# Kernel optimization log

Hardware: AMD Instinct MI355X
Metric: run time of the kernel (lower is better)

The kernel has to match this reference:

```python
import jax, jax.numpy as jnp
import numpy as np


def _ce(logits, labels):
    # per-element cross entropy; logits [N,C], labels [N] int
    logp = jax.nn.log_softmax(logits, axis=-1)
    return -jnp.take_along_axis(logp, labels[:, None].astype(jnp.int32), axis=1)[:, 0]


def _masked_mean(x, m):
    cnt = jnp.sum(m)
    return jnp.where(cnt > 0, jnp.sum(x * m) / jnp.maximum(cnt, 1.0), 0.0)


def _ohem(predict, target, train_mask, negative_ratio=3.0):
    # predict [N,2], target/train_mask [N] int {0,1}
    pos = (target * train_mask) > 0
    neg = ((1 - target) * train_mask) > 0
    n_pos = jnp.sum(pos).astype(jnp.float32)
    loss_all = _ce(predict, target)
    loss_pos = jnp.where(n_pos > 0, jnp.sum(jnp.where(pos, loss_all, 0.0)), 0.0)
    n_neg_total = jnp.sum(neg)
    n_neg = jnp.where(n_pos > 0,
                      jnp.minimum(n_neg_total, (negative_ratio * n_pos).astype(jnp.int32)),
                      jnp.minimum(100, n_neg_total))
    # hard-negative mining: top-n_neg of the per-pixel negative CE losses
    neg_sorted = jnp.sort(jnp.where(neg, loss_all, -jnp.inf))[::-1]
    loss_neg = jnp.sum(jnp.where(jnp.arange(neg_sorted.shape[0]) < n_neg, neg_sorted, 0.0))
    return (loss_pos + loss_neg) / (n_pos + n_neg.astype(jnp.float32))


def _forward(inputs, gcn_pred, gcn_labels, train_mask, tr_mask, tcl_mask, radii_map, sin_map, cos_map):
    B, C, H, W = inputs.shape
    ch = jnp.transpose(inputs, (0, 2, 3, 1)).reshape(-1, C)  # [N,8], N=B*H*W
    tr_pred = ch[:, 0:2]
    tcl_pred = ch[:, 2:4]
    sin_pred = ch[:, 4]
    cos_pred = ch[:, 5]
    scale = jnp.sqrt(1.0 / (sin_pred ** 2 + cos_pred ** 2 + 1e-4))
    sin_pred = sin_pred * scale
    cos_pred = cos_pred * scale
    top_pred = ch[:, 6]
    bot_pred = ch[:, 7]

    tm = train_mask.reshape(-1)
    tr = tr_mask.reshape(-1)
    tcl = tcl_mask[:, :, :, 0].reshape(-1)
    sin_t = sin_map.reshape(-1)
    cos_t = cos_map.reshape(-1)
    top_t = radii_map[:, :, :, 0].reshape(-1)
    bot_t = radii_map[:, :, :, 1].reshape(-1)

    # TR loss with OHEM hard-negative mining
    loss_tr = _ohem(tr_pred, tr, tm)

    # TCL loss: mean CE over train_mask*tr_mask positives
    tr_train = ((tm * tr) > 0).astype(jnp.float32)
    loss_tcl = _masked_mean(_ce(tcl_pred, tcl), tr_train)

    # geometry losses over tcl_mask pixels
    tclm = (tcl > 0).astype(jnp.float32)
    d_top = jnp.abs(top_pred / (top_t + 0.01) - 1.0)
    d_bot = jnp.abs(bot_pred / (bot_t + 0.01) - 1.0)
    sl_top = jnp.where(d_top < 1.0, 0.5 * d_top * d_top, d_top - 0.5)  # torch smooth_l1 (beta=1)
    sl_bot = jnp.where(d_bot < 1.0, 0.5 * d_bot * d_bot, d_bot - 0.5)
    loss_radii = _masked_mean(sl_top + sl_bot, tclm)

    sigma = 9.0
    d_sin = jnp.abs(sin_pred - sin_t)
    d_cos = jnp.abs(cos_pred - cos_t)
    sl_sin = jnp.where(d_sin < 1.0 / sigma, 0.5 * d_sin * d_sin * sigma, d_sin - 0.5 / sigma)
    sl_cos = jnp.where(d_cos < 1.0 / sigma, 0.5 * d_cos * d_cos * sigma, d_cos - 0.5 / sigma)
    loss_sin = _masked_mean(sl_sin, tclm)
    loss_cos = _masked_mean(sl_cos, tclm)

    gcn_loss = jnp.mean(_ce(gcn_pred, gcn_labels.reshape(-1)))
    return (loss_tr, loss_tcl, loss_sin, loss_cos, loss_radii, gcn_loss)


def setup_inputs() -> dict:
    key = jax.random.key(0)
    ks = jax.random.split(key, 9)
    B, H, W = 8, 640, 640
    return {
        'inputs': jax.random.normal(ks[0], (B, 8, H, W), dtype=jnp.float32),
        'gcn_pred': jax.random.normal(ks[1], (4096, 2), dtype=jnp.float32),
        'gcn_labels': jax.random.randint(ks[2], (4096,), 0, 2, dtype=jnp.int32),
        'train_mask': jax.random.randint(ks[3], (B, H, W), 0, 2, dtype=jnp.int32),
        'tr_mask': jax.random.randint(ks[4], (B, H, W), 0, 2, dtype=jnp.int32),
        'tcl_mask': jax.random.randint(ks[5], (B, H, W, 2), 0, 2, dtype=jnp.int32),
        'radii_map': jax.random.uniform(ks[6], (B, H, W, 2), dtype=jnp.float32),
        'sin_map': jax.random.normal(ks[7], (B, H, W), dtype=jnp.float32),
        'cos_map': jax.random.normal(ks[8], (B, H, W), dtype=jnp.float32),
    }


def reference(inputs, gcn_pred, gcn_labels, train_mask, tr_mask, tcl_mask, radii_map, sin_map, cos_map):
    return _forward(inputs, gcn_pred, gcn_labels, train_mask, tr_mask, tcl_mask, radii_map, sin_map, cos_map)
```

## Files before the change

### kernel.cpp

```cpp
#include <hip/hip_runtime.h>

#define HW_ 409600
#define NPIX 3276800
#define NB 4096
#define NGCN 4096
#define NBLK 2048

struct Ws {
  double sums[8];
  unsigned int cnts[8];
  unsigned int hcnt[NB];
  float hsum[NB];
  float pf[NBLK][8];
  unsigned int pc[NBLK][4];
};

__device__ __forceinline__ float ce2(float a0, float a1, int label) {
  float mx = fmaxf(a0, a1);
  float mn = fminf(a0, a1);
  float lse = mx + __logf(1.0f + __expf(mn - mx));
  return lse - (label ? a1 : a0);
}

__global__ __launch_bounds__(256) void k_init(Ws* ws) {
  int tid = threadIdx.x + blockIdx.x * blockDim.x;
  int nth = blockDim.x * gridDim.x;
  for (int i = tid; i < NB; i += nth) { ws->hcnt[i] = 0u; ws->hsum[i] = 0.f; }
}

__global__ __launch_bounds__(256) void k_main(
    const float* __restrict__ inp,
    const float* __restrict__ gcn_pred,
    const int* __restrict__ gcn_lab,
    const int* __restrict__ tmm,
    const int* __restrict__ trm,
    const int* __restrict__ tclm,
    const float* __restrict__ radm,
    const float* __restrict__ sinm,
    const float* __restrict__ cosm,
    Ws* __restrict__ ws) {
  float s_pos = 0.f, s_neg = 0.f, s_tcl = 0.f, s_sin = 0.f, s_cos = 0.f, s_rad = 0.f, s_gcn = 0.f;
  unsigned int c_pos = 0, c_neg = 0, c_tcl = 0;
  float mx_neg = 0.f;

  int tid = threadIdx.x + blockIdx.x * blockDim.x;
  int nth = blockDim.x * gridDim.x;

  if (tid < NGCN) {
    s_gcn = ce2(gcn_pred[2 * tid], gcn_pred[2 * tid + 1], gcn_lab[tid]);
  }

  const int ngrp = NPIX / 4;
  for (int g = tid; g < ngrp; g += nth) {
    int p = g * 4;
    int b = p / HW_;
    int q = p - b * HW_;
    const float* base = inp + (size_t)b * 8 * HW_ + q;
    float4 v0 = *(const float4*)(base);
    float4 v1 = *(const float4*)(base + HW_);
    float4 v2 = *(const float4*)(base + 2 * HW_);
    float4 v3 = *(const float4*)(base + 3 * HW_);
    float4 v4 = *(const float4*)(base + 4 * HW_);
    float4 v5 = *(const float4*)(base + 5 * HW_);
    float4 v6 = *(const float4*)(base + 6 * HW_);
    float4 v7 = *(const float4*)(base + 7 * HW_);
    int4 wtm = *(const int4*)(tmm + p);
    int4 wtr = *(const int4*)(trm + p);
    int4 tca = *(const int4*)(tclm + 2 * p);
    int4 tcb = *(const int4*)(tclm + 2 * p + 4);
    float4 ra = *(const float4*)(radm + 2 * p);
    float4 rb = *(const float4*)(radm + 2 * p + 4);
    float4 vs = *(const float4*)(sinm + p);
    float4 vc = *(const float4*)(cosm + p);

    float a0[4] = {v0.x, v0.y, v0.z, v0.w};
    float a1[4] = {v1.x, v1.y, v1.z, v1.w};
    float a2[4] = {v2.x, v2.y, v2.z, v2.w};
    float a3[4] = {v3.x, v3.y, v3.z, v3.w};
    float a4[4] = {v4.x, v4.y, v4.z, v4.w};
    float a5[4] = {v5.x, v5.y, v5.z, v5.w};
    float a6[4] = {v6.x, v6.y, v6.z, v6.w};
    float a7[4] = {v7.x, v7.y, v7.z, v7.w};
    int tmj[4] = {wtm.x, wtm.y, wtm.z, wtm.w};
    int trj[4] = {wtr.x, wtr.y, wtr.z, wtr.w};
    int tcj[4] = {tca.x, tca.z, tcb.x, tcb.z};
    float topt[4] = {ra.x, ra.z, rb.x, rb.z};
    float bott[4] = {ra.y, ra.w, rb.y, rb.w};
    float sint[4] = {vs.x, vs.y, vs.z, vs.w};
    float cost[4] = {vc.x, vc.y, vc.z, vc.w};

#pragma unroll
    for (int j = 0; j < 4; ++j) {
      bool pos = (trj[j] * tmj[j]) > 0;
      bool neg = ((1 - trj[j]) * tmj[j]) > 0;
      float ltr = ce2(a0[j], a1[j], trj[j]);
      if (pos) { s_pos += ltr; c_pos++; }
      if (neg) { s_neg += ltr; c_neg++; mx_neg = fmaxf(mx_neg, ltr); }
      float ltc = ce2(a2[j], a3[j], tcj[j]);
      if (pos) s_tcl += ltc;
      bool tc = tcj[j] > 0;
      float sp = a4[j], cp = a5[j];
      float sc = __builtin_amdgcn_rsqf(sp * sp + cp * cp + 1e-4f);
      sp *= sc; cp *= sc;
      float dsin = fabsf(sp - sint[j]);
      float dcos = fabsf(cp - cost[j]);
      const float inv9 = 1.f / 9.f;
      float slsin = dsin < inv9 ? 4.5f * dsin * dsin : dsin - 0.5f * inv9;
      float slcos = dcos < inv9 ? 4.5f * dcos * dcos : dcos - 0.5f * inv9;
      float dtop = fabsf(a6[j] * __builtin_amdgcn_rcpf(topt[j] + 0.01f) - 1.f);
      float dbot = fabsf(a7[j] * __builtin_amdgcn_rcpf(bott[j] + 0.01f) - 1.f);
      float sltop = dtop < 1.f ? 0.5f * dtop * dtop : dtop - 0.5f;
      float slbot = dbot < 1.f ? 0.5f * dbot * dbot : dbot - 0.5f;
      if (tc) { s_sin += slsin; s_cos += slcos; s_rad += sltop + slbot; c_tcl++; }
    }
  }

#pragma unroll
  for (int off = 32; off > 0; off >>= 1) {
    s_pos += __shfl_down(s_pos, off);
    s_neg += __shfl_down(s_neg, off);
    s_tcl += __shfl_down(s_tcl, off);
    s_sin += __shfl_down(s_sin, off);
    s_cos += __shfl_down(s_cos, off);
    s_rad += __shfl_down(s_rad, off);
    s_gcn += __shfl_down(s_gcn, off);
    c_pos += __shfl_down(c_pos, off);
    c_neg += __shfl_down(c_neg, off);
    c_tcl += __shfl_down(c_tcl, off);
    mx_neg = fmaxf(mx_neg, __shfl_down(mx_neg, off));
  }
  __shared__ float shf[4][8];
  __shared__ unsigned int shc[4][3];
  int wv = threadIdx.x >> 6, ln = threadIdx.x & 63;
  if (ln == 0) {
    shf[wv][0] = s_pos; shf[wv][1] = s_neg; shf[wv][2] = s_tcl; shf[wv][3] = s_sin;
    shf[wv][4] = s_cos; shf[wv][5] = s_rad; shf[wv][6] = s_gcn; shf[wv][7] = mx_neg;
    shc[wv][0] = c_pos; shc[wv][1] = c_neg; shc[wv][2] = c_tcl;
  }
  __syncthreads();
  if (threadIdx.x == 0) {
    float f0 = 0, f1 = 0, f2 = 0, f3 = 0, f4 = 0, f5 = 0, f6 = 0, f7 = 0;
    unsigned int u0 = 0, u1 = 0, u2 = 0;
#pragma unroll
    for (int w = 0; w < 4; ++w) {
      f0 += shf[w][0]; f1 += shf[w][1]; f2 += shf[w][2]; f3 += shf[w][3];
      f4 += shf[w][4]; f5 += shf[w][5]; f6 += shf[w][6];
      f7 = fmaxf(f7, shf[w][7]);
      u0 += shc[w][0]; u1 += shc[w][1]; u2 += shc[w][2];
    }
    ws->pf[blockIdx.x][0] = f0; ws->pf[blockIdx.x][1] = f1;
    ws->pf[blockIdx.x][2] = f2; ws->pf[blockIdx.x][3] = f3;
    ws->pf[blockIdx.x][4] = f4; ws->pf[blockIdx.x][5] = f5;
    ws->pf[blockIdx.x][6] = f6; ws->pf[blockIdx.x][7] = f7;
    ws->pc[blockIdx.x][0] = u0; ws->pc[blockIdx.x][1] = u1; ws->pc[blockIdx.x][2] = u2;
  }
}

__global__ __launch_bounds__(1024) void k_reduce(Ws* __restrict__ ws, float* __restrict__ out) {
  float f[8] = {0, 0, 0, 0, 0, 0, 0, 0};
  unsigned int u[3] = {0, 0, 0};
  int t = threadIdx.x;
#pragma unroll
  for (int rep = 0; rep < NBLK / 1024; ++rep) {
    int s = t + rep * 1024;
#pragma unroll
    for (int i = 0; i < 7; ++i) f[i] += ws->pf[s][i];
    f[7] = fmaxf(f[7], ws->pf[s][7]);
#pragma unroll
    for (int i = 0; i < 3; ++i) u[i] += ws->pc[s][i];
  }
#pragma unroll
  for (int off = 32; off > 0; off >>= 1) {
#pragma unroll
    for (int i = 0; i < 7; ++i) f[i] += __shfl_down(f[i], off);
    f[7] = fmaxf(f[7], __shfl_down(f[7], off));
#pragma unroll
    for (int i = 0; i < 3; ++i) u[i] += __shfl_down(u[i], off);
  }
  __shared__ float shf[16][8];
  __shared__ unsigned int shc[16][3];
  int wv = t >> 6, ln = t & 63;
  if (ln == 0) {
#pragma unroll
    for (int i = 0; i < 8; ++i) shf[wv][i] = f[i];
#pragma unroll
    for (int i = 0; i < 3; ++i) shc[wv][i] = u[i];
  }
  __syncthreads();
  if (t == 0) {
    double d[7] = {0, 0, 0, 0, 0, 0, 0};
    float mx = 0.f;
    unsigned int np = 0, nnt = 0, ntc = 0;
#pragma unroll
    for (int w = 0; w < 16; ++w) {
#pragma unroll
      for (int i = 0; i < 7; ++i) d[i] += (double)shf[w][i];
      mx = fmaxf(mx, shf[w][7]);
      np += shc[w][0]; nnt += shc[w][1]; ntc += shc[w][2];
    }
    ws->sums[0] = d[0];
    ws->cnts[0] = np;
    ws->cnts[5] = __float_as_uint(mx);
    out[1] = np > 0 ? (float)(d[2] / (double)np) : 0.f;
    out[2] = ntc > 0 ? (float)(d[3] / (double)ntc) : 0.f;
    out[3] = ntc > 0 ? (float)(d[4] / (double)ntc) : 0.f;
    out[4] = ntc > 0 ? (float)(d[5] / (double)ntc) : 0.f;
    out[5] = (float)(d[6] / (double)NGCN);
    long long nneg;
    if (np > 0) {
      long long cap = (long long)(int)(3.0f * (float)np);
      nneg = (long long)nnt < cap ? (long long)nnt : cap;
    } else {
      nneg = (long long)nnt < 100 ? (long long)nnt : 100;
    }
    if (nneg >= (long long)nnt) {
      out[0] = (float)((d[0] + d[1]) / ((double)np + (double)nneg));
      ws->cnts[3] = 0u;
    } else {
      ws->cnts[3] = 1u;
      ws->cnts[4] = (unsigned int)nneg;
    }
  }
}

__global__ __launch_bounds__(256) void k_hist(
    const float* __restrict__ inp,
    const int* __restrict__ tmm,
    const int* __restrict__ trm,
    Ws* __restrict__ ws) {
  if (ws->cnts[3] == 0u) return;
  __shared__ unsigned int lc[NB];
  __shared__ float lsum[NB];
  for (int i = threadIdx.x; i < NB; i += blockDim.x) { lc[i] = 0u; lsum[i] = 0.f; }
  __syncthreads();
  float maxneg = __uint_as_float(ws->cnts[5]);
  float invmax = maxneg > 0.f ? (float)NB / maxneg : 0.f;
  int tid = threadIdx.x + blockIdx.x * blockDim.x;
  int nth = blockDim.x * gridDim.x;
  for (int p = tid; p < NPIX; p += nth) {
    int tmj = tmm[p], trj = trm[p];
    if (((1 - trj) * tmj) > 0) {
      int b = p / HW_;
      int q = p - b * HW_;
      const float* base = inp + (size_t)b * 8 * HW_ + q;
      float ltr = ce2(base[0], base[HW_], trj);
      int bin = (int)(ltr * invmax);
      bin = bin < NB - 1 ? bin : NB - 1;
      bin = bin > 0 ? bin : 0;
      atomicAdd(&lc[bin], 1u);
      atomicAdd(&lsum[bin], ltr);
    }
  }
  __syncthreads();
  for (int i = threadIdx.x; i < NB; i += blockDim.x) {
    if (lc[i]) {
      atomicAdd(&ws->hcnt[i], lc[i]);
      atomicAdd(&ws->hsum[i], lsum[i]);
    }
  }
}

__global__ void k_fin2(Ws* __restrict__ ws, float* __restrict__ out) {
  if (threadIdx.x != 0 || blockIdx.x != 0) return;
  if (ws->cnts[3] == 0u) return;
  unsigned int k = ws->cnts[4];
  double acc = 0.0;
  unsigned int cum = 0;
  for (int b = NB - 1; b >= 0 && cum < k; --b) {
    unsigned int c = ws->hcnt[b];
    if (!c) continue;
    float s = ws->hsum[b];
    if (cum + c <= k) {
      acc += (double)s;
      cum += c;
    } else {
      unsigned int r = k - cum;
      acc += (double)r * ((double)s / (double)c);
      cum = k;
    }
  }
  unsigned int np = ws->cnts[0];
  double spos = ws->sums[0];
  out[0] = (float)((spos + acc) / ((double)np + (double)k));
}

extern "C" void kernel_launch(void* const* d_in, const int* in_sizes, int n_in,
                              void* d_out, int out_size, void* d_ws, size_t ws_size,
                              hipStream_t stream) {
  (void)in_sizes; (void)n_in; (void)out_size; (void)ws_size;
  const float* inp = (const float*)d_in[0];
  const float* gcn_pred = (const float*)d_in[1];
  const int* gcn_lab = (const int*)d_in[2];
  const int* tmm = (const int*)d_in[3];
  const int* trm = (const int*)d_in[4];
  const int* tclm = (const int*)d_in[5];
  const float* radm = (const float*)d_in[6];
  const float* sinm = (const float*)d_in[7];
  const float* cosm = (const float*)d_in[8];
  float* out = (float*)d_out;
  Ws* ws = (Ws*)d_ws;

  k_init<<<16, 256, 0, stream>>>(ws);
  k_main<<<NBLK, 256, 0, stream>>>(inp, gcn_pred, gcn_lab, tmm, trm, tclm, radm, sinm, cosm, ws);
  k_reduce<<<1, 1024, 0, stream>>>(ws, out);
  k_hist<<<256, 256, 0, stream>>>(inp, tmm, trm, ws);
  k_fin2<<<1, 64, 0, stream>>>(ws, out);
}
```

Measured before the change: 55.49 us.

## Use exact-fit grid with two prefetched pixel groups per thread and fold init into reduce

Sizes the main grid to 1600 blocks of 256 threads so each thread handles exactly two 4-pixel groups. Both groups' loads are issued before either is computed, which puts more memory requests in flight per thread and removes the grid-stride loop. The histogram zeroing kernel is removed and its work moved into the single-block reduce kernel, saving one launch. The fixed offset hardcodes the problem size, and the occupancy hint of 4 may constrain register allocation.

After: 54.99 us. No clear change (-0.9%).

```diff
diff --git a/kernel.cpp b/kernel.cpp
--- a/kernel.cpp
+++ b/kernel.cpp
@@ -4,7 +4,7 @@
 #define NPIX 3276800
 #define NB 4096
 #define NGCN 4096
-#define NBLK 2048
+#define NBLK 1600
 
 struct Ws {
   double sums[8];
@@ -22,57 +22,45 @@
   return lse - (label ? a1 : a0);
 }
 
-__global__ __launch_bounds__(256) void k_init(Ws* ws) {
-  int tid = threadIdx.x + blockIdx.x * blockDim.x;
-  int nth = blockDim.x * gridDim.x;
-  for (int i = tid; i < NB; i += nth) { ws->hcnt[i] = 0u; ws->hsum[i] = 0.f; }
-}
-
-__global__ __launch_bounds__(256) void k_main(
-    const float* __restrict__ inp,
-    const float* __restrict__ gcn_pred,
-    const int* __restrict__ gcn_lab,
-    const int* __restrict__ tmm,
-    const int* __restrict__ trm,
-    const int* __restrict__ tclm,
-    const float* __restrict__ radm,
-    const float* __restrict__ sinm,
-    const float* __restrict__ cosm,
-    Ws* __restrict__ ws) {
-  float s_pos = 0.f, s_neg = 0.f, s_tcl = 0.f, s_sin = 0.f, s_cos = 0.f, s_rad = 0.f, s_gcn = 0.f;
-  unsigned int c_pos = 0, c_neg = 0, c_tcl = 0;
-  float mx_neg = 0.f;
-
-  int tid = threadIdx.x + blockIdx.x * blockDim.x;
-  int nth = blockDim.x * gridDim.x;
-
-  if (tid < NGCN) {
-    s_gcn = ce2(gcn_pred[2 * tid], gcn_pred[2 * tid + 1], gcn_lab[tid]);
-  }
-
-  const int ngrp = NPIX / 4;
-  for (int g = tid; g < ngrp; g += nth) {
+struct Acc {
+  float s_pos, s_neg, s_tcl, s_sin, s_cos, s_rad;
+  unsigned int c_pos, c_neg, c_tcl;
+  float mx_neg;
+};
+
+struct Pack {
+  float4 v0, v1, v2, v3, v4, v5, v6, v7;
+  int4 wtm, wtr, tca, tcb;
+  float4 ra, rb, vs, vc;
+
+  __device__ __forceinline__ void load(
+      int g, const float* __restrict__ inp, const int* __restrict__ tmm,
+      const int* __restrict__ trm, const int* __restrict__ tclm,
+      const float* __restrict__ radm, const float* __restrict__ sinm,
+      const float* __restrict__ cosm) {
     int p = g * 4;
     int b = p / HW_;
     int q = p - b * HW_;
     const float* base = inp + (size_t)b * 8 * HW_ + q;
-    float4 v0 = *(const float4*)(base);
-    float4 v1 = *(const float4*)(base + HW_);
-    float4 v2 = *(const float4*)(base + 2 * HW_);
-    float4 v3 = *(const float4*)(base + 3 * HW_);
-    float4 v4 = *(const float4*)(base + 4 * HW_);
-    float4 v5 = *(const float4*)(base + 5 * HW_);
-    float4 v6 = *(const float4*)(base + 6 * HW_);
-    float4 v7 = *(const float4*)(base + 7 * HW_);
-    int4 wtm = *(const int4*)(tmm + p);
-    int4 wtr = *(const int4*)(trm + p);
-    int4 tca = *(const int4*)(tclm + 2 * p);
-    int4 tcb = *(const int4*)(tclm + 2 * p + 4);
-    float4 ra = *(const float4*)(radm + 2 * p);
-    float4 rb = *(const float4*)(radm + 2 * p + 4);
-    float4 vs = *(const float4*)(sinm + p);
-    float4 vc = *(const float4*)(cosm + p);
-
+    v0 = *(const float4*)(base);
+    v1 = *(const float4*)(base + HW_);
+    v2 = *(const float4*)(base + 2 * HW_);
+    v3 = *(const float4*)(base + 3 * HW_);
+    v4 = *(const float4*)(base + 4 * HW_);
+    v5 = *(const float4*)(base + 5 * HW_);
+    v6 = *(const float4*)(base + 6 * HW_);
+    v7 = *(const float4*)(base + 7 * HW_);
+    wtm = *(const int4*)(tmm + p);
+    wtr = *(const int4*)(trm + p);
+    tca = *(const int4*)(tclm + 2 * p);
+    tcb = *(const int4*)(tclm + 2 * p + 4);
+    ra = *(const float4*)(radm + 2 * p);
+    rb = *(const float4*)(radm + 2 * p + 4);
+    vs = *(const float4*)(sinm + p);
+    vc = *(const float4*)(cosm + p);
+  }
+
+  __device__ __forceinline__ void compute(Acc& a) {
     float a0[4] = {v0.x, v0.y, v0.z, v0.w};
     float a1[4] = {v1.x, v1.y, v1.z, v1.w};
     float a2[4] = {v2.x, v2.y, v2.z, v2.w};
@@ -88,16 +76,15 @@
     float bott[4] = {ra.y, ra.w, rb.y, rb.w};
     float sint[4] = {vs.x, vs.y, vs.z, vs.w};
     float cost[4] = {vc.x, vc.y, vc.z, vc.w};
-
 #pragma unroll
     for (int j = 0; j < 4; ++j) {
       bool pos = (trj[j] * tmj[j]) > 0;
       bool neg = ((1 - trj[j]) * tmj[j]) > 0;
       float ltr = ce2(a0[j], a1[j], trj[j]);
-      if (pos) { s_pos += ltr; c_pos++; }
-      if (neg) { s_neg += ltr; c_neg++; mx_neg = fmaxf(mx_neg, ltr); }
+      if (pos) { a.s_pos += ltr; a.c_pos++; }
+      if (neg) { a.s_neg += ltr; a.c_neg++; a.mx_neg = fmaxf(a.mx_neg, ltr); }
       float ltc = ce2(a2[j], a3[j], tcj[j]);
-      if (pos) s_tcl += ltc;
+      if (pos) a.s_tcl += ltc;
       bool tc = tcj[j] > 0;
       float sp = a4[j], cp = a5[j];
       float sc = __builtin_amdgcn_rsqf(sp * sp + cp * cp + 1e-4f);
@@ -111,31 +98,58 @@
       float dbot = fabsf(a7[j] * __builtin_amdgcn_rcpf(bott[j] + 0.01f) - 1.f);
       float sltop = dtop < 1.f ? 0.5f * dtop * dtop : dtop - 0.5f;
       float slbot = dbot < 1.f ? 0.5f * dbot * dbot : dbot - 0.5f;
-      if (tc) { s_sin += slsin; s_cos += slcos; s_rad += sltop + slbot; c_tcl++; }
-    }
-  }
+      if (tc) { a.s_sin += slsin; a.s_cos += slcos; a.s_rad += sltop + slbot; a.c_tcl++; }
+    }
+  }
+};
+
+__global__ __launch_bounds__(256, 4) void k_main(
+    const float* __restrict__ inp,
+    const float* __restrict__ gcn_pred,
+    const int* __restrict__ gcn_lab,
+    const int* __restrict__ tmm,
+    const int* __restrict__ trm,
+    const int* __restrict__ tclm,
+    const float* __restrict__ radm,
+    const float* __restrict__ sinm,
+    const float* __restrict__ cosm,
+    Ws* __restrict__ ws) {
+  Acc a = {0.f, 0.f, 0.f, 0.f, 0.f, 0.f, 0u, 0u, 0u, 0.f};
+  float s_gcn = 0.f;
+
+  int tid = threadIdx.x + blockIdx.x * blockDim.x;
+
+  if (tid < NGCN) {
+    s_gcn = ce2(gcn_pred[2 * tid], gcn_pred[2 * tid + 1], gcn_lab[tid]);
+  }
+
+  Pack A, B;
+  A.load(tid,          inp, tmm, trm, tclm, radm, sinm, cosm);
+  B.load(tid + 409600, inp, tmm, trm, tclm, radm, sinm, cosm);
+  A.compute(a);
+  B.compute(a);
 
 #pragma unroll
   for (int off = 32; off > 0; off >>= 1) {
-    s_pos += __shfl_down(s_pos, off);
-    s_neg += __shfl_down(s_neg, off);
-    s_tcl += __shfl_down(s_tcl, off);
-    s_sin += __shfl_down(s_sin, off);
-    s_cos += __shfl_down(s_cos, off);
-    s_rad += __shfl_down(s_rad, off);
-    s_gcn += __shfl_down(s_gcn, off);
-    c_pos += __shfl_down(c_pos, off);
-    c_neg += __shfl_down(c_neg, off);
-    c_tcl += __shfl_down(c_tcl, off);
-    mx_neg = fmaxf(mx_neg, __shfl_down(mx_neg, off));
+    a.s_pos += __shfl_down(a.s_pos, off);
+    a.s_neg += __shfl_down(a.s_neg, off);
+    a.s_tcl += __shfl_down(a.s_tcl, off);
+    a.s_sin += __shfl_down(a.s_sin, off);
+    a.s_cos += __shfl_down(a.s_cos, off);
+    a.s_rad += __shfl_down(a.s_rad, off);
+    s_gcn   += __shfl_down(s_gcn, off);
+    a.c_pos += __shfl_down(a.c_pos, off);
+    a.c_neg += __shfl_down(a.c_neg, off);
+    a.c_tcl += __shfl_down(a.c_tcl, off);
+    a.mx_neg = fmaxf(a.mx_neg, __shfl_down(a.mx_neg, off));
   }
   __shared__ float shf[4][8];
   __shared__ unsigned int shc[4][3];
   int wv = threadIdx.x >> 6, ln = threadIdx.x & 63;
   if (ln == 0) {
-    shf[wv][0] = s_pos; shf[wv][1] = s_neg; shf[wv][2] = s_tcl; shf[wv][3] = s_sin;
-    shf[wv][4] = s_cos; shf[wv][5] = s_rad; shf[wv][6] = s_gcn; shf[wv][7] = mx_neg;
-    shc[wv][0] = c_pos; shc[wv][1] = c_neg; shc[wv][2] = c_tcl;
+    shf[wv][0] = a.s_pos; shf[wv][1] = a.s_neg; shf[wv][2] = a.s_tcl; shf[wv][3] = a.s_sin;
+    shf[wv][4] = a.s_cos; shf[wv][5] = a.s_rad; shf[wv][6] = s_gcn;  shf[wv][7] = a.mx_neg;
+    shc[wv][0] = a.c_pos; shc[wv][1] = a.c_neg; shc[wv][2] = a.c_tcl;
   }
   __syncthreads();
   if (threadIdx.x == 0) {
@@ -157,17 +171,22 @@
 }
 
 __global__ __launch_bounds__(1024) void k_reduce(Ws* __restrict__ ws, float* __restrict__ out) {
+  int t = threadIdx.x;
+#pragma unroll
+  for (int i = t; i < NB; i += 1024) { ws->hcnt[i] = 0u; ws->hsum[i] = 0.f; }
+
   float f[8] = {0, 0, 0, 0, 0, 0, 0, 0};
   unsigned int u[3] = {0, 0, 0};
-  int t = threadIdx.x;
-#pragma unroll
-  for (int rep = 0; rep < NBLK / 1024; ++rep) {
+#pragma unroll
+  for (int rep = 0; rep < 2; ++rep) {
     int s = t + rep * 1024;
-#pragma unroll
-    for (int i = 0; i < 7; ++i) f[i] += ws->pf[s][i];
-    f[7] = fmaxf(f[7], ws->pf[s][7]);
-#pragma unroll
-    for (int i = 0; i < 3; ++i) u[i] += ws->pc[s][i];
+    if (s < NBLK) {
+#pragma unroll
+      for (int i = 0; i < 7; ++i) f[i] += ws->pf[s][i];
+      f[7] = fmaxf(f[7], ws->pf[s][7]);
+#pragma unroll
+      for (int i = 0; i < 3; ++i) u[i] += ws->pc[s][i];
+    }
   }
 #pragma unroll
   for (int off = 32; off > 0; off >>= 1) {
@@ -300,7 +319,6 @@
   float* out = (float*)d_out;
   Ws* ws = (Ws*)d_ws;
 
-  k_init<<<16, 256, 0, stream>>>(ws);
   k_main<<<NBLK, 256, 0, stream>>>(inp, gcn_pred, gcn_lab, tmm, trm, tclm, radm, sinm, cosm, ws);
   k_reduce<<<1, 1024, 0, stream>>>(ws, out);
   k_hist<<<256, 256, 0, stream>>>(inp, tmm, trm, ws);
```

## Fold reduce and finalize kernels into last-block epilogues and use nontemporal loads

Applied to the files above, without the earlier changes.

Replaces the separate init, reduce and final-selection kernels with last-block-done patterns: the last k_main block zeroes the histogram and does the global reduction, and the last k_hist block does the top-k walk. A small memset resets the completion counters. This cuts kernel launches and the gaps between them. Main-loop loads also switch to nontemporal loads to reduce cache pollution from the streaming data. The cost is a serialized tail in one block and reliance on atomics and fences for correctness.

Measured after the change: 145.5 us. 162% more time.

```diff
diff --git a/kernel.cpp b/kernel.cpp
--- a/kernel.cpp
+++ b/kernel.cpp
@@ -5,8 +5,15 @@
 #define NB 4096
 #define NGCN 4096
 #define NBLK 2048
+#define HBLK 256
+
+typedef float vf4 __attribute__((ext_vector_type(4)));
+typedef int vi4 __attribute__((ext_vector_type(4)));
 
 struct Ws {
+  unsigned int done;
+  unsigned int done2;
+  unsigned int pad[2];
   double sums[8];
   unsigned int cnts[8];
   unsigned int hcnt[NB];
@@ -22,10 +29,11 @@
   return lse - (label ? a1 : a0);
 }
 
-__global__ __launch_bounds__(256) void k_init(Ws* ws) {
-  int tid = threadIdx.x + blockIdx.x * blockDim.x;
-  int nth = blockDim.x * gridDim.x;
-  for (int i = tid; i < NB; i += nth) { ws->hcnt[i] = 0u; ws->hsum[i] = 0.f; }
+__device__ __forceinline__ vf4 ld4f(const float* p) {
+  return __builtin_nontemporal_load((const vf4*)p);
+}
+__device__ __forceinline__ vi4 ld4i(const int* p) {
+  return __builtin_nontemporal_load((const vi4*)p);
 }
 
 __global__ __launch_bounds__(256) void k_main(
@@ -38,7 +46,8 @@
     const float* __restrict__ radm,
     const float* __restrict__ sinm,
     const float* __restrict__ cosm,
-    Ws* __restrict__ ws) {
+    Ws* __restrict__ ws,
+    float* __restrict__ out) {
   float s_pos = 0.f, s_neg = 0.f, s_tcl = 0.f, s_sin = 0.f, s_cos = 0.f, s_rad = 0.f, s_gcn = 0.f;
   unsigned int c_pos = 0, c_neg = 0, c_tcl = 0;
   float mx_neg = 0.f;
@@ -56,22 +65,22 @@
     int b = p / HW_;
     int q = p - b * HW_;
     const float* base = inp + (size_t)b * 8 * HW_ + q;
-    float4 v0 = *(const float4*)(base);
-    float4 v1 = *(const float4*)(base + HW_);
-    float4 v2 = *(const float4*)(base + 2 * HW_);
-    float4 v3 = *(const float4*)(base + 3 * HW_);
-    float4 v4 = *(const float4*)(base + 4 * HW_);
-    float4 v5 = *(const float4*)(base + 5 * HW_);
-    float4 v6 = *(const float4*)(base + 6 * HW_);
-    float4 v7 = *(const float4*)(base + 7 * HW_);
-    int4 wtm = *(const int4*)(tmm + p);
-    int4 wtr = *(const int4*)(trm + p);
-    int4 tca = *(const int4*)(tclm + 2 * p);
-    int4 tcb = *(const int4*)(tclm + 2 * p + 4);
-    float4 ra = *(const float4*)(radm + 2 * p);
-    float4 rb = *(const float4*)(radm + 2 * p + 4);
-    float4 vs = *(const float4*)(sinm + p);
-    float4 vc = *(const float4*)(cosm + p);
+    vf4 v0 = ld4f(base);
+    vf4 v1 = ld4f(base + HW_);
+    vf4 v2 = ld4f(base + 2 * HW_);
+    vf4 v3 = ld4f(base + 3 * HW_);
+    vf4 v4 = ld4f(base + 4 * HW_);
+    vf4 v5 = ld4f(base + 5 * HW_);
+    vf4 v6 = ld4f(base + 6 * HW_);
+    vf4 v7 = ld4f(base + 7 * HW_);
+    vi4 wtm = ld4i(tmm + p);
+    vi4 wtr = ld4i(trm + p);
+    vi4 tca = ld4i(tclm + 2 * p);
+    vi4 tcb = ld4i(tclm + 2 * p + 4);
+    vf4 ra = ld4f(radm + 2 * p);
+    vf4 rb = ld4f(radm + 2 * p + 4);
+    vf4 vs = ld4f(sinm + p);
+    vf4 vc = ld4f(cosm + p);
 
     float a0[4] = {v0.x, v0.y, v0.z, v0.w};
     float a1[4] = {v1.x, v1.y, v1.z, v1.w};
@@ -131,6 +140,7 @@
   }
   __shared__ float shf[4][8];
   __shared__ unsigned int shc[4][3];
+  __shared__ unsigned int isLast;
   int wv = threadIdx.x >> 6, ln = threadIdx.x & 63;
   if (ln == 0) {
     shf[wv][0] = s_pos; shf[wv][1] = s_neg; shf[wv][2] = s_tcl; shf[wv][3] = s_sin;
@@ -153,72 +163,80 @@
     ws->pf[blockIdx.x][4] = f4; ws->pf[blockIdx.x][5] = f5;
     ws->pf[blockIdx.x][6] = f6; ws->pf[blockIdx.x][7] = f7;
     ws->pc[blockIdx.x][0] = u0; ws->pc[blockIdx.x][1] = u1; ws->pc[blockIdx.x][2] = u2;
-  }
-}
-
-__global__ __launch_bounds__(1024) void k_reduce(Ws* __restrict__ ws, float* __restrict__ out) {
-  float f[8] = {0, 0, 0, 0, 0, 0, 0, 0};
-  unsigned int u[3] = {0, 0, 0};
-  int t = threadIdx.x;
-#pragma unroll
-  for (int rep = 0; rep < NBLK / 1024; ++rep) {
-    int s = t + rep * 1024;
-#pragma unroll
-    for (int i = 0; i < 7; ++i) f[i] += ws->pf[s][i];
-    f[7] = fmaxf(f[7], ws->pf[s][7]);
-#pragma unroll
-    for (int i = 0; i < 3; ++i) u[i] += ws->pc[s][i];
-  }
-#pragma unroll
-  for (int off = 32; off > 0; off >>= 1) {
-#pragma unroll
-    for (int i = 0; i < 7; ++i) f[i] += __shfl_down(f[i], off);
-    f[7] = fmaxf(f[7], __shfl_down(f[7], off));
-#pragma unroll
-    for (int i = 0; i < 3; ++i) u[i] += __shfl_down(u[i], off);
-  }
-  __shared__ float shf[16][8];
-  __shared__ unsigned int shc[16][3];
-  int wv = t >> 6, ln = t & 63;
-  if (ln == 0) {
-#pragma unroll
-    for (int i = 0; i < 8; ++i) shf[wv][i] = f[i];
-#pragma unroll
-    for (int i = 0; i < 3; ++i) shc[wv][i] = u[i];
-  }
-  __syncthreads();
-  if (t == 0) {
-    double d[7] = {0, 0, 0, 0, 0, 0, 0};
-    float mx = 0.f;
-    unsigned int np = 0, nnt = 0, ntc = 0;
-#pragma unroll
-    for (int w = 0; w < 16; ++w) {
-#pragma unroll
-      for (int i = 0; i < 7; ++i) d[i] += (double)shf[w][i];
-      mx = fmaxf(mx, shf[w][7]);
-      np += shc[w][0]; nnt += shc[w][1]; ntc += shc[w][2];
-    }
-    ws->sums[0] = d[0];
-    ws->cnts[0] = np;
-    ws->cnts[5] = __float_as_uint(mx);
-    out[1] = np > 0 ? (float)(d[2] / (double)np) : 0.f;
-    out[2] = ntc > 0 ? (float)(d[3] / (double)ntc) : 0.f;
-    out[3] = ntc > 0 ? (float)(d[4] / (double)ntc) : 0.f;
-    out[4] = ntc > 0 ? (float)(d[5] / (double)ntc) : 0.f;
-    out[5] = (float)(d[6] / (double)NGCN);
-    long long nneg;
-    if (np > 0) {
-      long long cap = (long long)(int)(3.0f * (float)np);
-      nneg = (long long)nnt < cap ? (long long)nnt : cap;
-    } else {
-      nneg = (long long)nnt < 100 ? (long long)nnt : 100;
-    }
-    if (nneg >= (long long)nnt) {
-      out[0] = (float)((d[0] + d[1]) / ((double)np + (double)nneg));
-      ws->cnts[3] = 0u;
-    } else {
-      ws->cnts[3] = 1u;
-      ws->cnts[4] = (unsigned int)nneg;
+    __threadfence();
+    unsigned int old = atomicAdd(&ws->done, 1u);
+    isLast = (old == NBLK - 1) ? 1u : 0u;
+  }
+  __syncthreads();
+
+  if (isLast) {
+    __threadfence();
+    int t = threadIdx.x;
+#pragma unroll
+    for (int i = 0; i < NB / 256; ++i) { ws->hcnt[t + i * 256] = 0u; ws->hsum[t + i * 256] = 0.f; }
+
+    float f[8] = {0, 0, 0, 0, 0, 0, 0, 0};
+    unsigned int u[3] = {0, 0, 0};
+#pragma unroll
+    for (int rep = 0; rep < NBLK / 256; ++rep) {
+      int s = t + rep * 256;
+#pragma unroll
+      for (int i = 0; i < 7; ++i) f[i] += ws->pf[s][i];
+      f[7] = fmaxf(f[7], ws->pf[s][7]);
+#pragma unroll
+      for (int i = 0; i < 3; ++i) u[i] += ws->pc[s][i];
+    }
+#pragma unroll
+    for (int off = 32; off > 0; off >>= 1) {
+#pragma unroll
+      for (int i = 0; i < 7; ++i) f[i] += __shfl_down(f[i], off);
+      f[7] = fmaxf(f[7], __shfl_down(f[7], off));
+#pragma unroll
+      for (int i = 0; i < 3; ++i) u[i] += __shfl_down(u[i], off);
+    }
+    __shared__ float rf[4][8];
+    __shared__ unsigned int rc[4][3];
+    if (ln == 0) {
+#pragma unroll
+      for (int i = 0; i < 8; ++i) rf[wv][i] = f[i];
+#pragma unroll
+      for (int i = 0; i < 3; ++i) rc[wv][i] = u[i];
+    }
+    __syncthreads();
+    if (t == 0) {
+      double d[7] = {0, 0, 0, 0, 0, 0, 0};
+      float mx = 0.f;
+      unsigned int np = 0, nnt = 0, ntc = 0;
+#pragma unroll
+      for (int w = 0; w < 4; ++w) {
+#pragma unroll
+        for (int i = 0; i < 7; ++i) d[i] += (double)rf[w][i];
+        mx = fmaxf(mx, rf[w][7]);
+        np += rc[w][0]; nnt += rc[w][1]; ntc += rc[w][2];
+      }
+      ws->sums[0] = d[0];
+      ws->cnts[0] = np;
+      ws->cnts[5] = __float_as_uint(mx);
+      out[1] = np > 0 ? (float)(d[2] / (double)np) : 0.f;
+      out[2] = ntc > 0 ? (float)(d[3] / (double)ntc) : 0.f;
+      out[3] = ntc > 0 ? (float)(d[4] / (double)ntc) : 0.f;
+      out[4] = ntc > 0 ? (float)(d[5] / (double)ntc) : 0.f;
+      out[5] = (float)(d[6] / (double)NGCN);
+      long long nneg;
+      if (np > 0) {
+        long long cap = (long long)(int)(3.0f * (float)np);
+        nneg = (long long)nnt < cap ? (long long)nnt : cap;
+      } else {
+        nneg = (long long)nnt < 100 ? (long long)nnt : 100;
+      }
+      if (nneg >= (long long)nnt) {
+        out[0] = (float)((d[0] + d[1]) / ((double)np + (double)nneg));
+        ws->cnts[3] = 0u;
+      } else {
+        ws->cnts[3] = 1u;
+        ws->cnts[4] = (unsigned int)nneg;
+      }
+      __threadfence();
     }
   }
 }
@@ -227,7 +245,8 @@
     const float* __restrict__ inp,
     const int* __restrict__ tmm,
     const int* __restrict__ trm,
-    Ws* __restrict__ ws) {
+    Ws* __restrict__ ws,
+    float* __restrict__ out) {
   if (ws->cnts[3] == 0u) return;
   __shared__ unsigned int lc[NB];
   __shared__ float lsum[NB];
@@ -258,30 +277,36 @@
       atomicAdd(&ws->hsum[i], lsum[i]);
     }
   }
-}
-
-__global__ void k_fin2(Ws* __restrict__ ws, float* __restrict__ out) {
-  if (threadIdx.x != 0 || blockIdx.x != 0) return;
-  if (ws->cnts[3] == 0u) return;
-  unsigned int k = ws->cnts[4];
-  double acc = 0.0;
-  unsigned int cum = 0;
-  for (int b = NB - 1; b >= 0 && cum < k; --b) {
-    unsigned int c = ws->hcnt[b];
-    if (!c) continue;
-    float s = ws->hsum[b];
-    if (cum + c <= k) {
-      acc += (double)s;
-      cum += c;
-    } else {
-      unsigned int r = k - cum;
-      acc += (double)r * ((double)s / (double)c);
-      cum = k;
-    }
-  }
-  unsigned int np = ws->cnts[0];
-  double spos = ws->sums[0];
-  out[0] = (float)((spos + acc) / ((double)np + (double)k));
+  __shared__ unsigned int last2;
+  __threadfence();
+  __syncthreads();
+  if (threadIdx.x == 0) {
+    unsigned int old = atomicAdd(&ws->done2, 1u);
+    last2 = (old == HBLK - 1) ? 1u : 0u;
+  }
+  __syncthreads();
+  if (last2 && threadIdx.x == 0) {
+    __threadfence();
+    unsigned int k = ws->cnts[4];
+    double acc = 0.0;
+    unsigned int cum = 0;
+    for (int b = NB - 1; b >= 0 && cum < k; --b) {
+      unsigned int c = ws->hcnt[b];
+      if (!c) continue;
+      float s = ws->hsum[b];
+      if (cum + c <= k) {
+        acc += (double)s;
+        cum += c;
+      } else {
+        unsigned int r = k - cum;
+        acc += (double)r * ((double)s / (double)c);
+        cum = k;
+      }
+    }
+    unsigned int np = ws->cnts[0];
+    double spos = ws->sums[0];
+    out[0] = (float)((spos + acc) / ((double)np + (double)k));
+  }
 }
 
 extern "C" void kernel_launch(void* const* d_in, const int* in_sizes, int n_in,
@@ -300,9 +325,7 @@
   float* out = (float*)d_out;
   Ws* ws = (Ws*)d_ws;
 
-  k_init<<<16, 256, 0, stream>>>(ws);
-  k_main<<<NBLK, 256, 0, stream>>>(inp, gcn_pred, gcn_lab, tmm, trm, tclm, radm, sinm, cosm, ws);
-  k_reduce<<<1, 1024, 0, stream>>>(ws, out);
-  k_hist<<<256, 256, 0, stream>>>(inp, tmm, trm, ws);
-  k_fin2<<<1, 64, 0, stream>>>(ws, out);
-}
+  (void)hipMemsetAsync(d_ws, 0, 16, stream);
+  k_main<<<NBLK, 256, 0, stream>>>(inp, gcn_pred, gcn_lab, tmm, trm, tclm, radm, sinm, cosm, ws, out);
+  k_hist<<<HBLK, 256, 0, stream>>>(inp, tmm, trm, ws, out);
+}
```

## Drop init kernel, use one-pixel-group-per-thread main grid, shrink hist grid

Applied to the files above, without the earlier changes.

Removes the separate histogram-init kernel and folds the zeroing into the single-block reduce kernel, which saves one launch. The main kernel's grid becomes exactly NPIX/4/256 blocks, so each thread handles one 4-pixel group with no grid-stride loop, and the loads use ext_vector_type. The histogram kernel's grid drops from 256 to 64 blocks, which may cut atomic contention but also lowers parallelism. The partial-sum buffer in Ws must hold 3200 entries, so that depends on the workspace struct sizing with NBLK.

After: 49.22 us. 11.3% less time.

```diff
diff --git a/kernel.cpp b/kernel.cpp
--- a/kernel.cpp
+++ b/kernel.cpp
@@ -4,7 +4,11 @@
 #define NPIX 3276800
 #define NB 4096
 #define NGCN 4096
-#define NBLK 2048
+#define NBLK 3200
+#define HBLK 64
+
+typedef float vf4 __attribute__((ext_vector_type(4)));
+typedef int vi4 __attribute__((ext_vector_type(4)));
 
 struct Ws {
   double sums[8];
@@ -20,12 +24,6 @@
   float mn = fminf(a0, a1);
   float lse = mx + __logf(1.0f + __expf(mn - mx));
   return lse - (label ? a1 : a0);
-}
-
-__global__ __launch_bounds__(256) void k_init(Ws* ws) {
-  int tid = threadIdx.x + blockIdx.x * blockDim.x;
-  int nth = blockDim.x * gridDim.x;
-  for (int i = tid; i < NB; i += nth) { ws->hcnt[i] = 0u; ws->hsum[i] = 0.f; }
 }
 
 __global__ __launch_bounds__(256) void k_main(
@@ -44,34 +42,32 @@
   float mx_neg = 0.f;
 
   int tid = threadIdx.x + blockIdx.x * blockDim.x;
-  int nth = blockDim.x * gridDim.x;
 
   if (tid < NGCN) {
     s_gcn = ce2(gcn_pred[2 * tid], gcn_pred[2 * tid + 1], gcn_lab[tid]);
   }
 
-  const int ngrp = NPIX / 4;
-  for (int g = tid; g < ngrp; g += nth) {
-    int p = g * 4;
+  {
+    int p = tid * 4;
     int b = p / HW_;
     int q = p - b * HW_;
     const float* base = inp + (size_t)b * 8 * HW_ + q;
-    float4 v0 = *(const float4*)(base);
-    float4 v1 = *(const float4*)(base + HW_);
-    float4 v2 = *(const float4*)(base + 2 * HW_);
-    float4 v3 = *(const float4*)(base + 3 * HW_);
-    float4 v4 = *(const float4*)(base + 4 * HW_);
-    float4 v5 = *(const float4*)(base + 5 * HW_);
-    float4 v6 = *(const float4*)(base + 6 * HW_);
-    float4 v7 = *(const float4*)(base + 7 * HW_);
-    int4 wtm = *(const int4*)(tmm + p);
-    int4 wtr = *(const int4*)(trm + p);
-    int4 tca = *(const int4*)(tclm + 2 * p);
-    int4 tcb = *(const int4*)(tclm + 2 * p + 4);
-    float4 ra = *(const float4*)(radm + 2 * p);
-    float4 rb = *(const float4*)(radm + 2 * p + 4);
-    float4 vs = *(const float4*)(sinm + p);
-    float4 vc = *(const float4*)(cosm + p);
+    vf4 v0 = *(const vf4*)(base);
+    vf4 v1 = *(const vf4*)(base + HW_);
+    vf4 v2 = *(const vf4*)(base + 2 * HW_);
+    vf4 v3 = *(const vf4*)(base + 3 * HW_);
+    vf4 v4 = *(const vf4*)(base + 4 * HW_);
+    vf4 v5 = *(const vf4*)(base + 5 * HW_);
+    vf4 v6 = *(const vf4*)(base + 6 * HW_);
+    vf4 v7 = *(const vf4*)(base + 7 * HW_);
+    vi4 wtm = *(const vi4*)(tmm + p);
+    vi4 wtr = *(const vi4*)(trm + p);
+    vi4 tca = *(const vi4*)(tclm + 2 * p);
+    vi4 tcb = *(const vi4*)(tclm + 2 * p + 4);
+    vf4 ra = *(const vf4*)(radm + 2 * p);
+    vf4 rb = *(const vf4*)(radm + 2 * p + 4);
+    vf4 vs = *(const vf4*)(sinm + p);
+    vf4 vc = *(const vf4*)(cosm + p);
 
     float a0[4] = {v0.x, v0.y, v0.z, v0.w};
     float a1[4] = {v1.x, v1.y, v1.z, v1.w};
@@ -157,17 +153,22 @@
 }
 
 __global__ __launch_bounds__(1024) void k_reduce(Ws* __restrict__ ws, float* __restrict__ out) {
+  int t = threadIdx.x;
+#pragma unroll
+  for (int i = t; i < NB; i += 1024) { ws->hcnt[i] = 0u; ws->hsum[i] = 0.f; }
+
   float f[8] = {0, 0, 0, 0, 0, 0, 0, 0};
   unsigned int u[3] = {0, 0, 0};
-  int t = threadIdx.x;
-#pragma unroll
-  for (int rep = 0; rep < NBLK / 1024; ++rep) {
+#pragma unroll
+  for (int rep = 0; rep < (NBLK + 1023) / 1024; ++rep) {
     int s = t + rep * 1024;
-#pragma unroll
-    for (int i = 0; i < 7; ++i) f[i] += ws->pf[s][i];
-    f[7] = fmaxf(f[7], ws->pf[s][7]);
-#pragma unroll
-    for (int i = 0; i < 3; ++i) u[i] += ws->pc[s][i];
+    if (s < NBLK) {
+#pragma unroll
+      for (int i = 0; i < 7; ++i) f[i] += ws->pf[s][i];
+      f[7] = fmaxf(f[7], ws->pf[s][7]);
+#pragma unroll
+      for (int i = 0; i < 3; ++i) u[i] += ws->pc[s][i];
+    }
   }
 #pragma unroll
   for (int off = 32; off > 0; off >>= 1) {
@@ -300,9 +301,8 @@
   float* out = (float*)d_out;
   Ws* ws = (Ws*)d_ws;
 
-  k_init<<<16, 256, 0, stream>>>(ws);
   k_main<<<NBLK, 256, 0, stream>>>(inp, gcn_pred, gcn_lab, tmm, trm, tclm, radm, sinm, cosm, ws);
   k_reduce<<<1, 1024, 0, stream>>>(ws, out);
-  k_hist<<<256, 256, 0, stream>>>(inp, tmm, trm, ws);
+  k_hist<<<HBLK, 256, 0, stream>>>(inp, tmm, trm, ws);
   k_fin2<<<1, 64, 0, stream>>>(ws, out);
 }
```
